# Kernel optimization log

Measured on AMD Instinct MI355X. Metric: run time of the kernel, lower is better.

The kernel has to match this reference:

```python
import jax, jax.numpy as jnp
import numpy as np

TOP_K = 5
TEMPERATURE = 0.1
EPS = 1e-12


def _normalize(x):
    # F.normalize(x, dim=-1): x / max(||x||, eps)
    n = jnp.linalg.norm(x, axis=-1, keepdims=True)
    return x / jnp.maximum(n, EPS)


def setup_inputs() -> dict:
    key = jax.random.key(0)
    k1, k2, k3 = jax.random.split(key, 3)
    B, N, D = 1024, 200000, 128
    query = jax.random.normal(k1, (B, D), dtype=jnp.float32)
    # memory bank stores L2-normalized keys (MemoryBank.build applies F.normalize)
    memory = _normalize(jax.random.normal(k2, (N, D), dtype=jnp.float32))
    index_map = jnp.arange(N, dtype=jnp.int64)
    exclude_indices = jax.random.randint(k3, (B,), 0, N, dtype=jnp.int64)
    return {"query": query, "memory": memory, "index_map": index_map,
            "exclude_indices": exclude_indices}


def reference(query, memory, index_map, exclude_indices):
    # cosine similarity: normalize query, memory is already normalized
    qn = _normalize(query)                       # [B, D]
    sim = qn @ memory.T                          # [B, N]
    # exclude own training sample (training-time self-exclusion)
    mask = exclude_indices[:, None] == index_map[None, :]   # [B, N]
    sim = jnp.where(mask, -jnp.inf, sim)
    # top-k (effective_top_k = min(top_k, N-1) = TOP_K here)
    top_sim, top_idx = jax.lax.top_k(sim, TOP_K)             # [B, K]
    weights = jax.nn.softmax(top_sim / TEMPERATURE, axis=-1)  # [B, K]
    vecs = memory[top_idx]                                   # [B, K, D]
    retrieved = jnp.einsum('bk,bkd->bd', weights, vecs)      # weighted sum
    retrieved = _normalize(retrieved)
    distances = 1.0 - top_sim[:, 0]                          # [B]
    return retrieved, distances, weights
```

## Files before the change

### kernel.cpp

```cpp
#include <hip/hip_runtime.h>
#include <hip/hip_bf16.h>
#include <math.h>

#define D128 128
#define TOPK 5
#define NP 200704
#define NCH2 12544
#define NSTRIP 392
#define MARGIN 0.008f
#define CAP 1024
#define SCAP 96
#define SCST 44

typedef __attribute__((ext_vector_type(8))) short short8;
typedef __attribute__((ext_vector_type(4))) short s4v;
typedef __attribute__((ext_vector_type(4))) float f32x4;

__device__ __forceinline__ short f2bf(float f) {
    union { float f; unsigned u; } c; c.f = f;
    unsigned u = c.u + 0x7FFFu + ((c.u >> 16) & 1u);
    return (short)(u >> 16);
}

__device__ __forceinline__ unsigned pkbf(float x, float y) {
    __hip_bfloat162 h = __float22bfloat162_rn(make_float2(x, y));
    unsigned u; __builtin_memcpy(&u, &h, 4);
    return u;
}

template <int NN>
__device__ __forceinline__ void insertg(float (&v)[NN], int (&x)[NN], float nv, int nj) {
    bool g[NN];
    #pragma unroll
    for (int i = 0; i < NN; ++i) g[i] = nv > v[i];
    #pragma unroll
    for (int i = NN - 1; i > 0; --i) {
        v[i] = g[i - 1] ? v[i - 1] : (g[i] ? nv : v[i]);
        x[i] = g[i - 1] ? x[i - 1] : (g[i] ? nj : x[i]);
    }
    v[0] = g[0] ? nv : v[0];
    x[0] = g[0] ? nj : x[0];
}
template <int NN>
__device__ __forceinline__ void insertv(float (&v)[NN], float nv) {
    bool g[NN];
    #pragma unroll
    for (int i = 0; i < NN; ++i) g[i] = nv > v[i];
    #pragma unroll
    for (int i = NN - 1; i > 0; --i)
        v[i] = g[i - 1] ? v[i - 1] : (g[i] ? nv : v[i]);
    v[0] = g[0] ? nv : v[0];
}

__global__ void qnorm_kernel(const float* __restrict__ q, float* __restrict__ qn,
                             short* __restrict__ qbf) {
    int b = blockIdx.x, t = threadIdx.x;
    float v0 = q[(size_t)b * D128 + t];
    float v1 = q[(size_t)b * D128 + t + 64];
    float ss = v0 * v0 + v1 * v1;
    #pragma unroll
    for (int off = 32; off > 0; off >>= 1) ss += __shfl_xor(ss, off, 64);
    float scale = 1.0f / fmaxf(sqrtf(ss), 1e-12f);
    float a0 = v0 * scale, a1 = v1 * scale;
    qn[(size_t)b * D128 + t] = a0;
    qn[(size_t)b * D128 + t + 64] = a1;
    qbf[(size_t)b * D128 + t] = f2bf(a0);
    qbf[(size_t)b * D128 + t + 64] = f2bf(a1);
}

#define MFMA16(a, b, c) __builtin_amdgcn_mfma_f32_16x16x32_bf16(a, b, c, 0, 0, 0)

__global__ __launch_bounds__(256, 3) void simtopk_max(
    const short* __restrict__ qbf, const float* __restrict__ mem,
    _Float16* __restrict__ candT, _Float16* __restrict__ stripT, int N) {
    __shared__ short sK[64 * 136];
    __shared__ _Float16 sC[256 * SCST];
    const int b = blockIdx.x;
    const int strip = (b & 7) + ((b >> 5) << 3);
    const int qsg = (b >> 3) & 3;
    const int t = threadIdx.x, w = t >> 6, lane = t & 63;
    const int n = lane & 15, quad = lane >> 4;
    const bool qb0 = (quad & 1) != 0, qb1 = (quad & 2) != 0;
    const int qbase = qsg * 256 + w * 64;

    short8 bq[4][4];
    #pragma unroll
    for (int f = 0; f < 4; ++f) {
        const short* qrow = qbf + (size_t)(qbase + f * 16 + n) * D128 + quad * 8;
        #pragma unroll
        for (int s = 0; s < 4; ++s) bq[f][s] = *(const short8*)(qrow + s * 32);
    }

    const size_t k0 = (size_t)strip * 512;
    const int srow = t >> 4, scol = t & 15;
    const float* gbase = mem + (k0 + srow) * (size_t)D128 + scol * 8;
    const bool tail = (k0 + 512 > (size_t)N);

    float4 fa[8];

    auto loadg = [&](int g) {
        const float* base = gbase + (size_t)g * 64 * D128;
        #pragma unroll
        for (int i = 0; i < 4; ++i) {
            const float4* p = (const float4*)(base + (size_t)i * 16 * D128);
            if (tail) {
                size_t key = k0 + (size_t)(g * 64 + srow + i * 16);
                if (key >= (size_t)N) p = (const float4*)mem;
            }
            fa[2 * i]     = p[0];
            fa[2 * i + 1] = p[1];
        }
    };
    auto storesk = [&](int g) {
        #pragma unroll
        for (int i = 0; i < 4; ++i) {
            uint4 wv;
            wv.x = pkbf(fa[2 * i].x,     fa[2 * i].y);
            wv.y = pkbf(fa[2 * i].z,     fa[2 * i].w);
            wv.z = pkbf(fa[2 * i + 1].x, fa[2 * i + 1].y);
            wv.w = pkbf(fa[2 * i + 1].z, fa[2 * i + 1].w);
            if (tail && (k0 + (size_t)(g * 64 + srow + i * 16) >= (size_t)N))
                wv = make_uint4(0, 0, 0, 0);
            *((uint4*)&sK[(srow + 16 * i) * 136 + scol * 8]) = wv;
        }
    };

    loadg(0);
    storesk(0);
    __syncthreads();
    loadg(1);

    for (int round = 0; round < 8; ++round) {
        #pragma unroll
        for (int tt = 0; tt < 4; ++tt) {
            const short* ab = &sK[(tt * 16 + n) * 136 + quad * 8];
            short8 a0 = *(const short8*)(ab);
            short8 a1 = *(const short8*)(ab + 32);
            short8 a2 = *(const short8*)(ab + 64);
            short8 a3 = *(const short8*)(ab + 96);
            f32x4 c0 = {0.f, 0.f, 0.f, 0.f}, c1 = c0, c2 = c0, c3 = c0;
            c0 = MFMA16(a0, bq[0][0], c0);
            c1 = MFMA16(a0, bq[1][0], c1);
            c2 = MFMA16(a0, bq[2][0], c2);
            c3 = MFMA16(a0, bq[3][0], c3);
            c0 = MFMA16(a1, bq[0][1], c0);
            c1 = MFMA16(a1, bq[1][1], c1);
            c2 = MFMA16(a1, bq[2][1], c2);
            c3 = MFMA16(a1, bq[3][1], c3);
            c0 = MFMA16(a2, bq[0][2], c0);
            c1 = MFMA16(a2, bq[1][2], c1);
            c2 = MFMA16(a2, bq[2][2], c2);
            c3 = MFMA16(a2, bq[3][2], c3);
            c0 = MFMA16(a3, bq[0][3], c0);
            c1 = MFMA16(a3, bq[1][3], c1);
            c2 = MFMA16(a3, bq[2][3], c2);
            c3 = MFMA16(a3, bq[3][3], c3);
            float m0 = fmaxf(fmaxf(c0[0], c0[1]), fmaxf(c0[2], c0[3]));
            float m1 = fmaxf(fmaxf(c1[0], c1[1]), fmaxf(c1[2], c1[3]));
            float m2 = fmaxf(fmaxf(c2[0], c2[1]), fmaxf(c2[2], c2[3]));
            float m3 = fmaxf(fmaxf(c3[0], c3[1]), fmaxf(c3[2], c3[3]));
            float u0 = qb0 ? m1 : m0, u1 = qb0 ? m0 : m1;
            float u2 = qb0 ? m3 : m2, u3 = qb0 ? m2 : m3;
            float v0 = qb1 ? u2 : u0, v1 = qb1 ? u3 : u1;
            float v2 = qb1 ? u0 : u2, v3 = qb1 ? u1 : u3;
            float A = fmaxf(v0, __shfl_xor(v2, 32, 64));
            float B = fmaxf(v1, __shfl_xor(v3, 32, 64));
            float fin = fmaxf(A, __shfl_xor(B, 16, 64));
            sC[(w * 64 + quad * 16 + n) * SCST + round * 4 + tt] = (_Float16)fin;
        }
        if (round < 7) {
            __syncthreads();
            storesk(round + 1);
            __syncthreads();
            if (round < 6) loadg(round + 2);
        }
    }

    __syncthreads();
    {
        int q = qsg * 256 + t;
        short* dst = (short*)candT + (size_t)q * NCH2 + strip * 32;
        float mx = -3e38f;
        #pragma unroll
        for (int j = 0; j < 4; ++j) {
            s4v lo = *(const s4v*)(&sC[t * SCST + j * 8]);
            s4v hi = *(const s4v*)(&sC[t * SCST + j * 8 + 4]);
            short8 v;
            v[0] = lo[0]; v[1] = lo[1]; v[2] = lo[2]; v[3] = lo[3];
            v[4] = hi[0]; v[5] = hi[1]; v[6] = hi[2]; v[7] = hi[3];
            *(short8*)(dst + j * 8) = v;
            #pragma unroll
            for (int e = 0; e < 8; ++e) {
                short sv = v[e]; _Float16 hv; __builtin_memcpy(&hv, &sv, 2);
                mx = fmaxf(mx, (float)hv);
            }
        }
        stripT[(size_t)q * NSTRIP + strip] = (_Float16)mx;
    }
}

__global__ __launch_bounds__(256, 4) void finalize_batch(
    const _Float16* __restrict__ candT, const _Float16* __restrict__ stripT,
    const float* __restrict__ mem, const float* __restrict__ qn,
    const int* __restrict__ index_map, const int* __restrict__ excl,
    float* __restrict__ outR, float* __restrict__ outD, float* __restrict__ outW, int N) {
    const int q = blockIdx.x, t = threadIdx.x;
    const int w = t >> 6, lane = t & 63;

    __shared__ __align__(16) float sQ[D128];
    __shared__ __align__(16) _Float16 sS[NSTRIP];
    __shared__ unsigned short sStr[SCAP];
    __shared__ unsigned short sList[CAP];
    __shared__ int sScnt, sSov, sCnt, sOv;
    __shared__ float sThr;
    __shared__ float sMrg[4 * 6];
    __shared__ float sWv[4 * TOPK];
    __shared__ int   sWk[4 * TOPK];
    __shared__ float sW[TOPK];
    __shared__ int   sJ[TOPK];

    if (t < 128) sQ[t] = qn[(size_t)q * D128 + t];
    if (t == 0) { sScnt = 0; sSov = 0; sCnt = 0; sOv = 0; }
    if (t < NSTRIP / 8)
        *(short8*)(&sS[t * 8]) =
            *(const short8*)((const short*)stripT + (size_t)q * NSTRIP + t * 8);
    __syncthreads();

    float pv[6];
    #pragma unroll
    for (int i = 0; i < 6; ++i) pv[i] = -3e38f;
    for (int i = t; i < NSTRIP; i += 256) {
        float v = (float)sS[i];
        if (v > pv[5]) insertv<6>(pv, v);
    }
    #pragma unroll
    for (int r = 0; r < 6; ++r) {
        float bv = pv[0];
        #pragma unroll
        for (int off = 32; off > 0; off >>= 1) bv = fmaxf(bv, __shfl_xor(bv, off, 64));
        int ml = (pv[0] == bv) ? lane : 64;
        #pragma unroll
        for (int off = 32; off > 0; off >>= 1) ml = min(ml, __shfl_xor(ml, off, 64));
        if (lane == ml) {
            #pragma unroll
            for (int i = 0; i < 5; ++i) pv[i] = pv[i + 1];
            pv[5] = -3e38f;
        }
        if (lane == 0) sMrg[w * 6 + r] = bv;
    }
    __syncthreads();
    if (t == 0) {
        float b6[6];
        #pragma unroll
        for (int i = 0; i < 6; ++i) b6[i] = -3e38f;
        for (int j = 0; j < 24; ++j) {
            float v = sMrg[j];
            if (v > b6[5]) insertv<6>(b6, v);
        }
        sThr = b6[5] - 2.0f * MARGIN;
    }
    __syncthreads();

    const float thr = sThr;
    for (int i = t; i < NSTRIP; i += 256) {
        if ((float)sS[i] >= thr) {
            int p = atomicAdd(&sScnt, 1);
            if (p < SCAP) sStr[p] = (unsigned short)i; else sSov = 1;
        }
    }
    __syncthreads();
    const int scnt = min(sScnt, SCAP);

    if (!sSov) {
        for (int base = 0; base < scnt; base += 8) {
            int si = base + (t >> 5);
            if (si < scnt) {
                int ch = (int)sStr[si] * 32 + (t & 31);
                float v = (float)candT[(size_t)q * NCH2 + ch];
                if (v >= thr) {
                    int p = atomicAdd(&sCnt, 1);
                    if (p < CAP) sList[p] = (unsigned short)ch; else sOv = 1;
                }
            }
        }
    }
    __syncthreads();
    const int ov = (sSov || sOv) ? 1 : 0;
    const int cnt = ov ? NCH2 : min(sCnt, CAP);

    const int exq = excl[q];
    float tv[TOPK]; int ti[TOPK];
    #pragma unroll
    for (int i = 0; i < TOPK; ++i) { tv[i] = -3e38f; ti[i] = -1; }
    const int rounds = (cnt + 15) >> 4;
    for (int r = 0; r < rounds; ++r) {
        int slot = r * 16 + (t >> 4);
        int ch = (slot < cnt) ? (ov ? slot : (int)sList[slot]) : -1;
        int key = ch * 16 + (t & 15);
        float v = -3e38f;
        if (ch >= 0 && key < N && index_map[key] != exq) {
            const float4* mr = (const float4*)(mem + (size_t)key * D128);
            const float4* qv = (const float4*)sQ;
            float acc = 0.f;
            #pragma unroll
            for (int d = 0; d < 32; ++d) {
                float4 a = mr[d], b = qv[d];
                acc += a.x * b.x + a.y * b.y + a.z * b.z + a.w * b.w;
            }
            v = acc;
        }
        if (v > tv[TOPK - 1]) insertg<TOPK>(tv, ti, v, key);
    }

    #pragma unroll
    for (int r = 0; r < TOPK; ++r) {
        float bv = tv[0]; int bk = ti[0];
        #pragma unroll
        for (int off = 32; off > 0; off >>= 1) {
            float ovv = __shfl_xor(bv, off, 64);
            int   okk = __shfl_xor(bk, off, 64);
            if (ovv > bv || (ovv == bv && (unsigned)okk < (unsigned)bk)) { bv = ovv; bk = okk; }
        }
        if (tv[0] == bv && ti[0] == bk) {
            #pragma unroll
            for (int i = 0; i < TOPK - 1; ++i) { tv[i] = tv[i + 1]; ti[i] = ti[i + 1]; }
            tv[TOPK - 1] = -3e38f; ti[TOPK - 1] = -1;
        }
        if (lane == 0) { sWv[w * TOPK + r] = bv; sWk[w * TOPK + r] = bk; }
    }
    __syncthreads();
    if (t == 0) {
        float bv[TOPK]; int bi[TOPK];
        #pragma unroll
        for (int i = 0; i < TOPK; ++i) { bv[i] = -3e38f; bi[i] = -1; }
        for (int j = 0; j < 4 * TOPK; ++j) {
            float v = sWv[j];
            if (v > bv[TOPK - 1]) insertg<TOPK>(bv, bi, v, sWk[j]);
        }
        float m = bv[0], ex[TOPK], sum = 0.f;
        #pragma unroll
        for (int k = 0; k < TOPK; ++k) { ex[k] = __expf((bv[k] - m) * 10.0f); sum += ex[k]; }
        float inv = 1.0f / sum;
        #pragma unroll
        for (int k = 0; k < TOPK; ++k) {
            float wk = ex[k] * inv;
            sW[k] = wk; sJ[k] = bi[k];
            outW[(size_t)q * TOPK + k] = wk;
        }
        outD[q] = 1.0f - bv[0];
    }
    __syncthreads();
    if (t < 64) {
        float r0 = 0.f, r1 = 0.f;
        #pragma unroll
        for (int k = 0; k < TOPK; ++k) {
            const float* mr = mem + (size_t)sJ[k] * D128;
            r0 += sW[k] * mr[t];
            r1 += sW[k] * mr[t + 64];
        }
        float ss = r0 * r0 + r1 * r1;
        #pragma unroll
        for (int off = 32; off > 0; off >>= 1) ss += __shfl_xor(ss, off, 64);
        float scale = 1.0f / fmaxf(sqrtf(ss), 1e-12f);
        outR[(size_t)q * D128 + t]      = r0 * scale;
        outR[(size_t)q * D128 + t + 64] = r1 * scale;
    }
}

extern "C" void kernel_launch(void* const* d_in, const int* in_sizes, int n_in,
                              void* d_out, int out_size, void* d_ws, size_t ws_size,
                              hipStream_t stream) {
    const float* query  = (const float*)d_in[0];
    const float* memory = (const float*)d_in[1];
    const int* index_map = (const int*)d_in[2];
    const int* excl      = (const int*)d_in[3];

    const int B = in_sizes[3];
    const int N = in_sizes[2];

    char* ws = (char*)d_ws;
    float*    qn     = (float*)(ws);
    short*    qbf    = (short*)(ws + 524288);
    _Float16* candT  = (_Float16*)(ws + 786432);
    _Float16* stripT = (_Float16*)(ws + 786432 + 25690112);

    float* outR = (float*)d_out;
    float* outD = outR + (size_t)B * D128;
    float* outW = outD + B;

    qnorm_kernel<<<B, 64, 0, stream>>>(query, qn, qbf);
    simtopk_max<<<NSTRIP * 4, 256, 0, stream>>>(qbf, memory, candT, stripT, N);
    finalize_batch<<<B, 256, 0, stream>>>(candT, stripT, memory, qn, index_map, excl,
                                          outR, outD, outW, N);
}
```

Baseline: 247.0 us.

## Double-buffer shared key tile and pack candidate max writes in sim kernel

Adds a second shared-memory buffer for the bf16 key tile, so the next group is converted and stored while the current one feeds the MFMAs. This cuts the two barriers per round down to one. The four per-round fp16 maxima are now packed into two 32-bit shared stores, with a tighter sC row stride, and read back as dword loads for the global copy. The cost is double the sK shared memory, which may reduce occupancy under the 3-blocks-per-CU launch bound, and more live registers.

```diff
diff --git a/kernel.cpp b/kernel.cpp
--- a/kernel.cpp
+++ b/kernel.cpp
@@ -10,10 +10,9 @@
 #define MARGIN 0.008f
 #define CAP 1024
 #define SCAP 96
-#define SCST 44
+#define SCST 34
 
 typedef __attribute__((ext_vector_type(8))) short short8;
-typedef __attribute__((ext_vector_type(4))) short s4v;
 typedef __attribute__((ext_vector_type(4))) float f32x4;
 
 __device__ __forceinline__ short f2bf(float f) {
@@ -26,6 +25,10 @@
     __hip_bfloat162 h = __float22bfloat162_rn(make_float2(x, y));
     unsigned u; __builtin_memcpy(&u, &h, 4);
     return u;
+}
+__device__ __forceinline__ unsigned pkh(float a, float b) {
+    union { _Float16 h[2]; unsigned u; } c;
+    c.h[0] = (_Float16)a; c.h[1] = (_Float16)b; return c.u;
 }
 
 template <int NN>
@@ -73,7 +76,7 @@
 __global__ __launch_bounds__(256, 3) void simtopk_max(
     const short* __restrict__ qbf, const float* __restrict__ mem,
     _Float16* __restrict__ candT, _Float16* __restrict__ stripT, int N) {
-    __shared__ short sK[64 * 136];
+    __shared__ short sK[2][64 * 136];
     __shared__ _Float16 sC[256 * SCST];
     const int b = blockIdx.x;
     const int strip = (b & 7) + ((b >> 5) << 3);
@@ -111,7 +114,7 @@
             fa[2 * i + 1] = p[1];
         }
     };
-    auto storesk = [&](int g) {
+    auto storesk = [&](int g, int buf) {
         #pragma unroll
         for (int i = 0; i < 4; ++i) {
             uint4 wv;
@@ -121,19 +124,27 @@
             wv.w = pkbf(fa[2 * i + 1].z, fa[2 * i + 1].w);
             if (tail && (k0 + (size_t)(g * 64 + srow + i * 16) >= (size_t)N))
                 wv = make_uint4(0, 0, 0, 0);
-            *((uint4*)&sK[(srow + 16 * i) * 136 + scol * 8]) = wv;
+            *((uint4*)&sK[buf][(srow + 16 * i) * 136 + scol * 8]) = wv;
         }
     };
 
     loadg(0);
-    storesk(0);
+    storesk(0, 0);
     __syncthreads();
     loadg(1);
 
+    const int qloc = w * 64 + quad * 16 + n;
+    unsigned* sCrow = (unsigned*)((char*)sC + qloc * (SCST * 2));
+
     for (int round = 0; round < 8; ++round) {
+        if (round < 7) storesk(round + 1, (round + 1) & 1);
+        if (round < 6) loadg(round + 2);
+
+        const short* kb = sK[round & 1];
+        float fin[4];
         #pragma unroll
         for (int tt = 0; tt < 4; ++tt) {
-            const short* ab = &sK[(tt * 16 + n) * 136 + quad * 8];
+            const short* ab = &kb[(tt * 16 + n) * 136 + quad * 8];
             short8 a0 = *(const short8*)(ab);
             short8 a1 = *(const short8*)(ab + 32);
             short8 a2 = *(const short8*)(ab + 64);
@@ -165,34 +176,32 @@
             float v2 = qb1 ? u0 : u2, v3 = qb1 ? u1 : u3;
             float A = fmaxf(v0, __shfl_xor(v2, 32, 64));
             float B = fmaxf(v1, __shfl_xor(v3, 32, 64));
-            float fin = fmaxf(A, __shfl_xor(B, 16, 64));
-            sC[(w * 64 + quad * 16 + n) * SCST + round * 4 + tt] = (_Float16)fin;
-        }
-        if (round < 7) {
-            __syncthreads();
-            storesk(round + 1);
-            __syncthreads();
-            if (round < 6) loadg(round + 2);
-        }
-    }
-
-    __syncthreads();
+            fin[tt] = fmaxf(A, __shfl_xor(B, 16, 64));
+        }
+        sCrow[round * 2]     = pkh(fin[0], fin[1]);
+        sCrow[round * 2 + 1] = pkh(fin[2], fin[3]);
+        __syncthreads();
+    }
+
     {
         int q = qsg * 256 + t;
-        short* dst = (short*)candT + (size_t)q * NCH2 + strip * 32;
+        unsigned* gdst = (unsigned*)((short*)candT + (size_t)q * NCH2 + strip * 32);
+        const unsigned* row = (const unsigned*)((const char*)sC + t * (SCST * 2));
         float mx = -3e38f;
         #pragma unroll
         for (int j = 0; j < 4; ++j) {
-            s4v lo = *(const s4v*)(&sC[t * SCST + j * 8]);
-            s4v hi = *(const s4v*)(&sC[t * SCST + j * 8 + 4]);
-            short8 v;
-            v[0] = lo[0]; v[1] = lo[1]; v[2] = lo[2]; v[3] = lo[3];
-            v[4] = hi[0]; v[5] = hi[1]; v[6] = hi[2]; v[7] = hi[3];
-            *(short8*)(dst + j * 8) = v;
+            unsigned u0 = row[4 * j], u1 = row[4 * j + 1];
+            unsigned u2 = row[4 * j + 2], u3 = row[4 * j + 3];
+            uint4 v; v.x = u0; v.y = u1; v.z = u2; v.w = u3;
+            *(uint4*)(gdst + 4 * j) = v;
+            unsigned uu[4] = {u0, u1, u2, u3};
             #pragma unroll
-            for (int e = 0; e < 8; ++e) {
-                short sv = v[e]; _Float16 hv; __builtin_memcpy(&hv, &sv, 2);
-                mx = fmaxf(mx, (float)hv);
+            for (int e = 0; e < 4; ++e) {
+                unsigned short ha = (unsigned short)(uu[e] & 0xffff);
+                unsigned short hb = (unsigned short)(uu[e] >> 16);
+                _Float16 f0, f1;
+                __builtin_memcpy(&f0, &ha, 2); __builtin_memcpy(&f1, &hb, 2);
+                mx = fmaxf(mx, fmaxf((float)f0, (float)f1));
             }
         }
         stripT[(size_t)q * NSTRIP + strip] = (_Float16)mx;
```

Result: no change. 247.1 us (+0.0%).

## Load memory keys directly into MFMA registers, dropping LDS staging and barriers

Applied to the files above, without the earlier changes.

Each wave now loads its own 16-row key tile from global memory straight into registers in the MFMA operand layout, converts it to bf16 in place and prefetches the next tile. This removes the shared-memory key tile, the two block barriers per round and the LDS staging of per-chunk maxima. Results are written directly to global memory one fp16 at a time per row. The cost is that all four waves load the same key rows, so global/L2 traffic per block goes up fourfold, and the output stores become scattered 2-byte writes instead of 16-byte vector stores.

```diff
diff --git a/kernel.cpp b/kernel.cpp
--- a/kernel.cpp
+++ b/kernel.cpp
@@ -10,10 +10,8 @@
 #define MARGIN 0.008f
 #define CAP 1024
 #define SCAP 96
-#define SCST 44
 
 typedef __attribute__((ext_vector_type(8))) short short8;
-typedef __attribute__((ext_vector_type(4))) short s4v;
 typedef __attribute__((ext_vector_type(4))) float f32x4;
 
 __device__ __forceinline__ short f2bf(float f) {
@@ -26,6 +24,9 @@
     __hip_bfloat162 h = __float22bfloat162_rn(make_float2(x, y));
     unsigned u; __builtin_memcpy(&u, &h, 4);
     return u;
+}
+__device__ __forceinline__ short8 u4s8(uint4 u) {
+    short8 r; __builtin_memcpy(&r, &u, 16); return r;
 }
 
 template <int NN>
@@ -73,8 +74,6 @@
 __global__ __launch_bounds__(256, 3) void simtopk_max(
     const short* __restrict__ qbf, const float* __restrict__ mem,
     _Float16* __restrict__ candT, _Float16* __restrict__ stripT, int N) {
-    __shared__ short sK[64 * 136];
-    __shared__ _Float16 sC[256 * SCST];
     const int b = blockIdx.x;
     const int strip = (b & 7) + ((b >> 5) << 3);
     const int qsg = (b >> 3) & 3;
@@ -82,6 +81,7 @@
     const int n = lane & 15, quad = lane >> 4;
     const bool qb0 = (quad & 1) != 0, qb1 = (quad & 2) != 0;
     const int qbase = qsg * 256 + w * 64;
+    const int myq = qbase + quad * 16 + n;
 
     short8 bq[4][4];
     #pragma unroll
@@ -92,111 +92,66 @@
     }
 
     const size_t k0 = (size_t)strip * 512;
-    const int srow = t >> 4, scol = t & 15;
-    const float* gbase = mem + (k0 + srow) * (size_t)D128 + scol * 8;
     const bool tail = (k0 + 512 > (size_t)N);
-
-    float4 fa[8];
-
-    auto loadg = [&](int g) {
-        const float* base = gbase + (size_t)g * 64 * D128;
-        #pragma unroll
-        for (int i = 0; i < 4; ++i) {
-            const float4* p = (const float4*)(base + (size_t)i * 16 * D128);
-            if (tail) {
-                size_t key = k0 + (size_t)(g * 64 + srow + i * 16);
-                if (key >= (size_t)N) p = (const float4*)mem;
-            }
-            fa[2 * i]     = p[0];
-            fa[2 * i + 1] = p[1];
+    const float* abase = mem + (k0 + n) * (size_t)D128 + quad * 8;
+
+    float4 ta[8];
+    auto issue = [&](int r) {
+        const float4* p = (const float4*)(abase + (size_t)r * 16 * D128);
+        if (tail && (k0 + (size_t)(r * 16 + n) >= (size_t)N))
+            p = (const float4*)mem;
+        #pragma unroll
+        for (int s = 0; s < 4; ++s) {
+            ta[2 * s]     = p[s * 8];
+            ta[2 * s + 1] = p[s * 8 + 1];
         }
     };
-    auto storesk = [&](int g) {
-        #pragma unroll
-        for (int i = 0; i < 4; ++i) {
-            uint4 wv;
-            wv.x = pkbf(fa[2 * i].x,     fa[2 * i].y);
-            wv.y = pkbf(fa[2 * i].z,     fa[2 * i].w);
-            wv.z = pkbf(fa[2 * i + 1].x, fa[2 * i + 1].y);
-            wv.w = pkbf(fa[2 * i + 1].z, fa[2 * i + 1].w);
-            if (tail && (k0 + (size_t)(g * 64 + srow + i * 16) >= (size_t)N))
-                wv = make_uint4(0, 0, 0, 0);
-            *((uint4*)&sK[(srow + 16 * i) * 136 + scol * 8]) = wv;
+    auto cvt = [&](uint4 (&af)[4], int r) {
+        const bool zero = tail && (k0 + (size_t)(r * 16 + n) >= (size_t)N);
+        #pragma unroll
+        for (int s = 0; s < 4; ++s) {
+            uint4 u;
+            u.x = pkbf(ta[2 * s].x,     ta[2 * s].y);
+            u.y = pkbf(ta[2 * s].z,     ta[2 * s].w);
+            u.z = pkbf(ta[2 * s + 1].x, ta[2 * s + 1].y);
+            u.w = pkbf(ta[2 * s + 1].z, ta[2 * s + 1].w);
+            if (zero) u = make_uint4(0, 0, 0, 0);
+            af[s] = u;
         }
     };
 
-    loadg(0);
-    storesk(0);
-    __syncthreads();
-    loadg(1);
-
-    for (int round = 0; round < 8; ++round) {
-        #pragma unroll
-        for (int tt = 0; tt < 4; ++tt) {
-            const short* ab = &sK[(tt * 16 + n) * 136 + quad * 8];
-            short8 a0 = *(const short8*)(ab);
-            short8 a1 = *(const short8*)(ab + 32);
-            short8 a2 = *(const short8*)(ab + 64);
-            short8 a3 = *(const short8*)(ab + 96);
-            f32x4 c0 = {0.f, 0.f, 0.f, 0.f}, c1 = c0, c2 = c0, c3 = c0;
-            c0 = MFMA16(a0, bq[0][0], c0);
-            c1 = MFMA16(a0, bq[1][0], c1);
-            c2 = MFMA16(a0, bq[2][0], c2);
-            c3 = MFMA16(a0, bq[3][0], c3);
-            c0 = MFMA16(a1, bq[0][1], c0);
-            c1 = MFMA16(a1, bq[1][1], c1);
-            c2 = MFMA16(a1, bq[2][1], c2);
-            c3 = MFMA16(a1, bq[3][1], c3);
-            c0 = MFMA16(a2, bq[0][2], c0);
-            c1 = MFMA16(a2, bq[1][2], c1);
-            c2 = MFMA16(a2, bq[2][2], c2);
-            c3 = MFMA16(a2, bq[3][2], c3);
-            c0 = MFMA16(a3, bq[0][3], c0);
-            c1 = MFMA16(a3, bq[1][3], c1);
-            c2 = MFMA16(a3, bq[2][3], c2);
-            c3 = MFMA16(a3, bq[3][3], c3);
-            float m0 = fmaxf(fmaxf(c0[0], c0[1]), fmaxf(c0[2], c0[3]));
-            float m1 = fmaxf(fmaxf(c1[0], c1[1]), fmaxf(c1[2], c1[3]));
-            float m2 = fmaxf(fmaxf(c2[0], c2[1]), fmaxf(c2[2], c2[3]));
-            float m3 = fmaxf(fmaxf(c3[0], c3[1]), fmaxf(c3[2], c3[3]));
-            float u0 = qb0 ? m1 : m0, u1 = qb0 ? m0 : m1;
-            float u2 = qb0 ? m3 : m2, u3 = qb0 ? m2 : m3;
-            float v0 = qb1 ? u2 : u0, v1 = qb1 ? u3 : u1;
-            float v2 = qb1 ? u0 : u2, v3 = qb1 ? u1 : u3;
-            float A = fmaxf(v0, __shfl_xor(v2, 32, 64));
-            float B = fmaxf(v1, __shfl_xor(v3, 32, 64));
-            float fin = fmaxf(A, __shfl_xor(B, 16, 64));
-            sC[(w * 64 + quad * 16 + n) * SCST + round * 4 + tt] = (_Float16)fin;
-        }
-        if (round < 7) {
-            __syncthreads();
-            storesk(round + 1);
-            __syncthreads();
-            if (round < 6) loadg(round + 2);
-        }
-    }
-
-    __syncthreads();
-    {
-        int q = qsg * 256 + t;
-        short* dst = (short*)candT + (size_t)q * NCH2 + strip * 32;
-        float mx = -3e38f;
-        #pragma unroll
-        for (int j = 0; j < 4; ++j) {
-            s4v lo = *(const s4v*)(&sC[t * SCST + j * 8]);
-            s4v hi = *(const s4v*)(&sC[t * SCST + j * 8 + 4]);
-            short8 v;
-            v[0] = lo[0]; v[1] = lo[1]; v[2] = lo[2]; v[3] = lo[3];
-            v[4] = hi[0]; v[5] = hi[1]; v[6] = hi[2]; v[7] = hi[3];
-            *(short8*)(dst + j * 8) = v;
-            #pragma unroll
-            for (int e = 0; e < 8; ++e) {
-                short sv = v[e]; _Float16 hv; __builtin_memcpy(&hv, &sv, 2);
-                mx = fmaxf(mx, (float)hv);
-            }
-        }
-        stripT[(size_t)q * NSTRIP + strip] = (_Float16)mx;
-    }
+    issue(0);
+    float mx = -3e38f;
+    _Float16* crow = candT + (size_t)myq * NCH2 + strip * 32;
+
+    for (int r = 0; r < 32; ++r) {
+        uint4 af[4];
+        cvt(af, r);
+        if (r < 31) issue(r + 1);
+        f32x4 c0 = {0.f, 0.f, 0.f, 0.f}, c1 = c0, c2 = c0, c3 = c0;
+        #pragma unroll
+        for (int s = 0; s < 4; ++s) {
+            short8 a = u4s8(af[s]);
+            c0 = MFMA16(a, bq[0][s], c0);
+            c1 = MFMA16(a, bq[1][s], c1);
+            c2 = MFMA16(a, bq[2][s], c2);
+            c3 = MFMA16(a, bq[3][s], c3);
+        }
+        float m0 = fmaxf(fmaxf(c0[0], c0[1]), fmaxf(c0[2], c0[3]));
+        float m1 = fmaxf(fmaxf(c1[0], c1[1]), fmaxf(c1[2], c1[3]));
+        float m2 = fmaxf(fmaxf(c2[0], c2[1]), fmaxf(c2[2], c2[3]));
+        float m3 = fmaxf(fmaxf(c3[0], c3[1]), fmaxf(c3[2], c3[3]));
+        float u0 = qb0 ? m1 : m0, u1 = qb0 ? m0 : m1;
+        float u2 = qb0 ? m3 : m2, u3 = qb0 ? m2 : m3;
+        float v0 = qb1 ? u2 : u0, v1 = qb1 ? u3 : u1;
+        float v2 = qb1 ? u0 : u2, v3 = qb1 ? u1 : u3;
+        float A = fmaxf(v0, __shfl_xor(v2, 32, 64));
+        float B = fmaxf(v1, __shfl_xor(v3, 32, 64));
+        float fin = fmaxf(A, __shfl_xor(B, 16, 64));
+        crow[r] = (_Float16)fin;
+        mx = fmaxf(mx, fin);
+    }
+    stripT[(size_t)myq * NSTRIP + strip] = (_Float16)mx;
 }
 
 __global__ __launch_bounds__(256, 4) void finalize_batch(
```

New measurement: 543.4 us. +120.0%, slower.

## Double key span per block and remap block order for memory locality

Applied to the files above, without the earlier changes.

Each similarity block now covers 1024 memory keys (two strips) instead of 512, so the grid is halved. This amortises the per-block query fragment loads and prologue over twice as many keys. The block-to-(key group, query subgroup) mapping is permuted so the four query subgroups of one key group launch close together, and the smem candidate buffer is reused across the two halves with a mid-loop flush. Candidate maxima are now packed two halves per 32-bit shared store. The cost is fewer blocks (784) for the GPU to spread its load over, and a longer serial loop per block.

```diff
diff --git a/kernel.cpp b/kernel.cpp
--- a/kernel.cpp
+++ b/kernel.cpp
@@ -7,13 +7,13 @@
 #define NP 200704
 #define NCH2 12544
 #define NSTRIP 392
+#define NKG 196
 #define MARGIN 0.008f
 #define CAP 1024
 #define SCAP 96
-#define SCST 44
+#define SCST 34
 
 typedef __attribute__((ext_vector_type(8))) short short8;
-typedef __attribute__((ext_vector_type(4))) short s4v;
 typedef __attribute__((ext_vector_type(4))) float f32x4;
 
 __device__ __forceinline__ short f2bf(float f) {
@@ -26,6 +26,10 @@
     __hip_bfloat162 h = __float22bfloat162_rn(make_float2(x, y));
     unsigned u; __builtin_memcpy(&u, &h, 4);
     return u;
+}
+__device__ __forceinline__ unsigned pkh(float a, float b) {
+    union { _Float16 h[2]; unsigned u; } c;
+    c.h[0] = (_Float16)a; c.h[1] = (_Float16)b; return c.u;
 }
 
 template <int NN>
@@ -76,8 +80,9 @@
     __shared__ short sK[64 * 136];
     __shared__ _Float16 sC[256 * SCST];
     const int b = blockIdx.x;
-    const int strip = (b & 7) + ((b >> 5) << 3);
-    const int qsg = (b >> 3) & 3;
+    const int m = (b & 7) * 98 + (b >> 3);
+    const int kg = m >> 2;
+    const int qsg = m & 3;
     const int t = threadIdx.x, w = t >> 6, lane = t & 63;
     const int n = lane & 15, quad = lane >> 4;
     const bool qb0 = (quad & 1) != 0, qb1 = (quad & 2) != 0;
@@ -91,10 +96,10 @@
         for (int s = 0; s < 4; ++s) bq[f][s] = *(const short8*)(qrow + s * 32);
     }
 
-    const size_t k0 = (size_t)strip * 512;
+    const size_t k0 = (size_t)kg * 1024;
     const int srow = t >> 4, scol = t & 15;
     const float* gbase = mem + (k0 + srow) * (size_t)D128 + scol * 8;
-    const bool tail = (k0 + 512 > (size_t)N);
+    const bool tail = (k0 + 1024 > (size_t)N);
 
     float4 fa[8];
 
@@ -124,13 +129,50 @@
             *((uint4*)&sK[(srow + 16 * i) * 136 + scol * 8]) = wv;
         }
     };
+    auto flush = [&](int h) {
+        int q = qsg * 256 + t;
+        unsigned* gdst = (unsigned*)((short*)candT + (size_t)q * NCH2
+                                     + kg * 64 + h * 32);
+        const unsigned* row = (const unsigned*)((const char*)sC + t * (SCST * 2));
+        float mx = -3e38f;
+        uint4 v0, v1;
+        v0.x = row[0]; v0.y = row[1]; v0.z = row[2]; v0.w = row[3];
+        v1.x = row[4]; v1.y = row[5]; v1.z = row[6]; v1.w = row[7];
+        unsigned u8[8] = {v0.x, v0.y, v0.z, v0.w, v1.x, v1.y, v1.z, v1.w};
+        uint4 v2, v3;
+        v2.x = row[8];  v2.y = row[9];  v2.z = row[10]; v2.w = row[11];
+        v3.x = row[12]; v3.y = row[13]; v3.z = row[14]; v3.w = row[15];
+        unsigned u8b[8] = {v2.x, v2.y, v2.z, v2.w, v3.x, v3.y, v3.z, v3.w};
+        *(uint4*)(gdst)      = v0;
+        *(uint4*)(gdst + 4)  = v1;
+        *(uint4*)(gdst + 8)  = v2;
+        *(uint4*)(gdst + 12) = v3;
+        #pragma unroll
+        for (int e = 0; e < 8; ++e) {
+            unsigned ua = u8[e], ub = u8b[e];
+            unsigned short h0 = (unsigned short)(ua & 0xffff);
+            unsigned short h1 = (unsigned short)(ua >> 16);
+            unsigned short h2 = (unsigned short)(ub & 0xffff);
+            unsigned short h3 = (unsigned short)(ub >> 16);
+            _Float16 f0, f1, f2, f3;
+            __builtin_memcpy(&f0, &h0, 2); __builtin_memcpy(&f1, &h1, 2);
+            __builtin_memcpy(&f2, &h2, 2); __builtin_memcpy(&f3, &h3, 2);
+            mx = fmaxf(mx, fmaxf(fmaxf((float)f0, (float)f1),
+                                 fmaxf((float)f2, (float)f3)));
+        }
+        stripT[(size_t)q * NSTRIP + kg * 2 + h] = (_Float16)mx;
+    };
 
     loadg(0);
     storesk(0);
     __syncthreads();
     loadg(1);
 
-    for (int round = 0; round < 8; ++round) {
+    const int qloc = w * 64 + quad * 16 + n;
+    unsigned* sCrow = (unsigned*)((char*)sC + qloc * (SCST * 2));
+
+    for (int round = 0; round < 16; ++round) {
+        float fin[4];
         #pragma unroll
         for (int tt = 0; tt < 4; ++tt) {
             const short* ab = &sK[(tt * 16 + n) * 136 + quad * 8];
@@ -165,38 +207,21 @@
             float v2 = qb1 ? u0 : u2, v3 = qb1 ? u1 : u3;
             float A = fmaxf(v0, __shfl_xor(v2, 32, 64));
             float B = fmaxf(v1, __shfl_xor(v3, 32, 64));
-            float fin = fmaxf(A, __shfl_xor(B, 16, 64));
-            sC[(w * 64 + quad * 16 + n) * SCST + round * 4 + tt] = (_Float16)fin;
-        }
-        if (round < 7) {
+            fin[tt] = fmaxf(A, __shfl_xor(B, 16, 64));
+        }
+        sCrow[(round & 7) * 2]     = pkh(fin[0], fin[1]);
+        sCrow[(round & 7) * 2 + 1] = pkh(fin[2], fin[3]);
+        if (round < 15) {
             __syncthreads();
             storesk(round + 1);
+            if (round == 7) flush(0);
             __syncthreads();
-            if (round < 6) loadg(round + 2);
-        }
-    }
-
-    __syncthreads();
-    {
-        int q = qsg * 256 + t;
-        short* dst = (short*)candT + (size_t)q * NCH2 + strip * 32;
-        float mx = -3e38f;
-        #pragma unroll
-        for (int j = 0; j < 4; ++j) {
-            s4v lo = *(const s4v*)(&sC[t * SCST + j * 8]);
-            s4v hi = *(const s4v*)(&sC[t * SCST + j * 8 + 4]);
-            short8 v;
-            v[0] = lo[0]; v[1] = lo[1]; v[2] = lo[2]; v[3] = lo[3];
-            v[4] = hi[0]; v[5] = hi[1]; v[6] = hi[2]; v[7] = hi[3];
-            *(short8*)(dst + j * 8) = v;
-            #pragma unroll
-            for (int e = 0; e < 8; ++e) {
-                short sv = v[e]; _Float16 hv; __builtin_memcpy(&hv, &sv, 2);
-                mx = fmaxf(mx, (float)hv);
-            }
-        }
-        stripT[(size_t)q * NSTRIP + strip] = (_Float16)mx;
-    }
+            if (round < 14) loadg(round + 2);
+        }
+    }
+
+    __syncthreads();
+    flush(1);
 }
 
 __global__ __launch_bounds__(256, 4) void finalize_batch(
@@ -389,7 +414,7 @@
     float* outW = outD + B;
 
     qnorm_kernel<<<B, 64, 0, stream>>>(query, qn, qbf);
-    simtopk_max<<<NSTRIP * 4, 256, 0, stream>>>(qbf, memory, candT, stripT, N);
+    simtopk_max<<<NKG * 4, 256, 0, stream>>>(qbf, memory, candT, stripT, N);
     finalize_batch<<<B, 256, 0, stream>>>(candT, stripT, memory, qn, index_map, excl,
                                           outR, outD, outW, N);
 }
```

After: 252.3 us. +2.1%, slower.
